# Kernel tuning notes

Hardware: AMD Instinct MI355X
Metric: run time of the kernel (lower is better)

Reference implementation:

```python
import jax, jax.numpy as jnp
import numpy as np

B, T, C, H = 4, 2048, 1024, 16
D = C // H  # head dim = 64


def setup_inputs() -> dict:
    key = jax.random.key(0)
    ks = jax.random.split(key, 5)
    s = 1.0 / np.sqrt(C)
    return {
        "x": jax.random.normal(ks[0], (B, T, C), jnp.float32),
        "Wq": jax.random.normal(ks[1], (C, C), jnp.float32) * s,
        "bq": jnp.zeros((C,), jnp.float32),
        "Wk": jax.random.normal(ks[2], (C, C), jnp.float32) * s,
        "bk": jnp.zeros((C,), jnp.float32),
        "Wv": jax.random.normal(ks[3], (C, C), jnp.float32) * s,
        "bv": jnp.zeros((C,), jnp.float32),
        "Wp": jax.random.normal(ks[4], (C, C), jnp.float32) * s,
        "bp": jnp.zeros((C,), jnp.float32),
    }


def reference(x, Wq, bq, Wk, bk, Wv, bv, Wp, bp):
    # linear projections -> [B, H, T, D]
    def heads(t):
        return t.reshape(B, T, H, D).transpose(0, 2, 1, 3)
    q = heads(x @ Wq.T + bq)
    k = heads(x @ Wk.T + bk)
    v = heads(x @ Wv.T + bv)
    scale = 1.0 / np.sqrt(D)
    att = jnp.einsum("bhtd,bhsd->bhts", q, k) * scale  # [B,H,T,T]
    causal = jnp.tril(jnp.ones((T, T), bool))
    att = jnp.where(causal[None, None], att, -jnp.inf)
    att = jax.nn.softmax(att, axis=-1)
    y = jnp.einsum("bhts,bhsd->bhtd", att, v)  # [B,H,T,D]
    y = y.transpose(0, 2, 1, 3).reshape(B, T, C)
    return y @ Wp.T + bp
```

## Files before the change

kernel.cpp:

```cpp
#include <hip/hip_runtime.h>

typedef float f32x4 __attribute__((ext_vector_type(4)));
typedef float f32x16 __attribute__((ext_vector_type(16)));
typedef __bf16 bf16x8 __attribute__((ext_vector_type(8)));
typedef unsigned short u16x8 __attribute__((ext_vector_type(8)));

#define SCQ 0.1803368801111183f

__device__ inline unsigned short f2bf(float f) {
  unsigned int u = __builtin_bit_cast(unsigned int, f);
  u += 0x7FFFu + ((u >> 16) & 1u);
  return (unsigned short)(u >> 16);
}
__device__ inline unsigned short f2bf_fast(float f) {
  unsigned int u = __builtin_bit_cast(unsigned int, f);
  return (unsigned short)((u + 0x8000u) >> 16);
}

__device__ inline float fexp2(float x) {
#if __has_builtin(__builtin_amdgcn_exp2f)
  return __builtin_amdgcn_exp2f(x);
#else
  return exp2f(x);
#endif
}

template <int N>
__device__ inline float rowror(float v) {
  return __builtin_bit_cast(float, __builtin_amdgcn_update_dpp(
      0, __builtin_bit_cast(int, v), 0x120 | N, 0xF, 0xF, true));
}
__device__ inline float rowsum16(float v) {
  v += rowror<8>(v); v += rowror<4>(v);
  v += rowror<2>(v); v += rowror<1>(v);
  return v;
}

__device__ inline void gload_lds16(const unsigned short* g, unsigned short* l) {
  __builtin_amdgcn_global_load_lds(
      (const __attribute__((address_space(1))) unsigned int*)g,
      (__attribute__((address_space(3))) unsigned int*)l, 16, 0, 0);
}

__global__ void cvt_x(const float* __restrict__ in, unsigned short* __restrict__ out) {
  int i = (blockIdx.x * 256 + threadIdx.x) * 4;
  float4 f = *(const float4*)(in + i);
  ushort4 o;
  o.x = f2bf(f.x); o.y = f2bf(f.y); o.z = f2bf(f.z); o.w = f2bf(f.w);
  *(ushort4*)(out + i) = o;
}

__global__ void cvt_w(const float* __restrict__ a, const float* __restrict__ b,
                      const float* __restrict__ c, const float* __restrict__ d,
                      unsigned short* __restrict__ oa, unsigned short* __restrict__ ob,
                      unsigned short* __restrict__ oc, unsigned short* __restrict__ od) {
  const float* src[4] = {a, b, c, d};
  unsigned short* dst[4] = {oa, ob, oc, od};
  int m = blockIdx.y;
  int i = (blockIdx.x * 256 + threadIdx.x) * 4;
  float4 f = *(const float4*)(src[m] + i);
  ushort4 o;
  o.x = f2bf(f.x); o.y = f2bf(f.y); o.z = f2bf(f.z); o.w = f2bf(f.w);
  *(ushort4*)(dst[m] + i) = o;
}

template <int MODE>
__global__ __launch_bounds__(256) void gemm128(const unsigned short* __restrict__ A,
                                               const unsigned short* __restrict__ Bt,
                                               const float* __restrict__ b0,
                                               const float* __restrict__ b1,
                                               const float* __restrict__ b2,
                                               void* __restrict__ out,
                                               int M, int N, int K) {
  __shared__ __align__(16) unsigned short As[128 * 64];
  __shared__ __align__(16) unsigned short Bs[128 * 64];
  const int tid = threadIdx.x;
  const int lane = tid & 63, w = tid >> 6;
  const int l31 = lane & 31, half = lane >> 5;
  const int wm = w & 1, wn = w >> 1;
  const int m0 = blockIdx.x * 128, n0 = blockIdx.y * 128;

  f32x16 acc[2][2] = {};

  for (int kb = 0; kb < K; kb += 64) {
#pragma unroll
    for (int j = 0; j < 4; j++) {
      int ch = j * 256 + w * 64 + lane;
      int row = ch >> 3, pc = ch & 7;
      int c = pc ^ (row & 7);
      gload_lds16(A + (size_t)(m0 + row) * K + kb + c * 8, As + (size_t)(j * 256 + w * 64) * 8);
      gload_lds16(Bt + (size_t)(n0 + row) * K + kb + c * 8, Bs + (size_t)(j * 256 + w * 64) * 8);
    }
    __syncthreads();
#pragma unroll
    for (int ks = 0; ks < 64; ks += 16) {
      bf16x8 af[2], bfr[2];
#pragma unroll
      for (int at = 0; at < 2; at++) {
        int row = wm * 64 + at * 32 + l31;
        int pc = ((ks >> 3) + half) ^ (row & 7);
        af[at] = *(const bf16x8*)(As + row * 64 + pc * 8);
      }
#pragma unroll
      for (int nt = 0; nt < 2; nt++) {
        int row = wn * 64 + nt * 32 + l31;
        int pc = ((ks >> 3) + half) ^ (row & 7);
        bfr[nt] = *(const bf16x8*)(Bs + row * 64 + pc * 8);
      }
#pragma unroll
      for (int at = 0; at < 2; at++)
#pragma unroll
        for (int nt = 0; nt < 2; nt++)
          acc[at][nt] = __builtin_amdgcn_mfma_f32_32x32x16_bf16(af[at], bfr[nt], acc[at][nt], 0, 0, 0);
    }
    __syncthreads();
  }

#pragma unroll
  for (int at = 0; at < 2; at++)
#pragma unroll
    for (int nt = 0; nt < 2; nt++) {
      int col = n0 + wn * 64 + nt * 32 + l31;
      float bv, sc;
      int which = 0, cl = col;
      if (MODE == 0) {
        which = col >> 10; cl = col & 1023;
        const float* bp = (which == 0) ? b0 : ((which == 1) ? b1 : b2);
        bv = bp[cl];
        sc = (which == 0) ? SCQ : 1.f;
      } else {
        bv = b0[col]; sc = 1.f;
      }
#pragma unroll
      for (int reg = 0; reg < 16; reg++) {
        int row = m0 + wm * 64 + at * 32 + (reg & 3) + 8 * (reg >> 2) + 4 * half;
        float v = (acc[at][nt][reg] + bv) * sc;
        if (MODE == 0) {
          int h = cl >> 6, d = cl & 63;
          int b = row >> 11, t = row & 2047;
          ((unsigned short*)out)[(size_t)which * 8388608 +
                                 ((size_t)((b * 16 + h) * 2048 + t)) * 64 + d] = f2bf(v);
        } else {
          ((float*)out)[(size_t)row * N + col] = v;
        }
      }
    }
}

__global__ __launch_bounds__(256) void transpose_v(const unsigned short* __restrict__ V,
                                                   unsigned short* __restrict__ Vt) {
  constexpr int P = 66;
  __shared__ unsigned short L[64 * P];
  const int tid = threadIdx.x;
  const int bh = blockIdx.y;
  const int t0 = blockIdx.x * 64;
  const unsigned short* Vp = V + (size_t)bh * 2048 * 64;
  unsigned short* Op = Vt + (size_t)bh * 64 * 2048;
#pragma unroll
  for (int j = 0; j < 2; j++) {
    int r = (tid >> 3) + j * 32;
    int c = (tid & 7) * 8;
    u16x8 v = *(const u16x8*)(Vp + (size_t)(t0 + r) * 64 + c);
#pragma unroll
    for (int i = 0; i < 4; i++) {
      unsigned int pk = (unsigned int)v[2 * i] | ((unsigned int)v[2 * i + 1] << 16);
      *(unsigned int*)&L[r * P + c + 2 * i] = pk;
    }
  }
  __syncthreads();
#pragma unroll
  for (int j = 0; j < 2; j++) {
    int ch = j * 256 + tid;
    int d = ch >> 3, tc = (ch & 7) * 8;
    u16x8 o;
#pragma unroll
    for (int k = 0; k < 8; k++) o[k] = L[(tc + k) * P + d];
    *(u16x8*)(Op + (size_t)d * 2048 + t0 + tc) = o;
  }
}

#define PPITCH 72
__device__ __attribute__((always_inline)) inline
void attn_tile(int qt, int s0, const bf16x8* aq, const unsigned short* Ks,
               const unsigned short* Vs, unsigned short* pl,
               f32x4* o, float* lrow, int quad, int l15) {
  const bool full = (s0 + 63) <= qt;
  const int nsc = full ? 4 : (((qt + 15 - s0) >> 4) + 1);
  const int nsc2 = (nsc + 1) & ~1;

#pragma unroll
  for (int sc = 0; sc < 4; sc++) {
    if (sc < nsc) {
      f32x4 s = {};
#pragma unroll
      for (int kh = 0; kh < 2; kh++) {
        int kr = sc * 16 + l15;
        int pc = (kh * 4 + quad) ^ (kr & 7);
        u16x8 bku = *(const u16x8*)(Ks + kr * 64 + pc * 8);
        s = __builtin_amdgcn_mfma_f32_16x16x32_bf16(aq[kh], __builtin_bit_cast(bf16x8, bku), s, 0, 0, 0);
      }
      if (full) {
#pragma unroll
        for (int r = 0; r < 4; r++) {
          float e = fexp2(s[r]);
          lrow[r] += e;
          pl[(quad * 4 + r) * PPITCH + sc * 16 + l15] = f2bf_fast(e);
        }
      } else {
        int sg = s0 + sc * 16 + l15;
#pragma unroll
        for (int r = 0; r < 4; r++) {
          float e = fexp2(s[r]);
          e = (sg > qt + quad * 4 + r) ? 0.f : e;
          lrow[r] += e;
          pl[(quad * 4 + r) * PPITCH + sc * 16 + l15] = f2bf_fast(e);
        }
      }
    } else if (sc < nsc2) {
#pragma unroll
      for (int r = 0; r < 4; r++)
        pl[(quad * 4 + r) * PPITCH + sc * 16 + l15] = 0;
    }
  }
  __asm__ __volatile__("" ::: "memory");
#pragma unroll
  for (int h2 = 0; h2 < 2; h2++) {
    if (h2 * 2 < nsc2) {
      u16x8 apu = *(const u16x8*)(pl + l15 * PPITCH + h2 * 32 + quad * 8);
      bf16x8 ap = __builtin_bit_cast(bf16x8, apu);
#pragma unroll
      for (int dc = 0; dc < 4; dc++) {
        int vr = dc * 16 + l15;
        int pc = (h2 * 4 + quad) ^ (vr & 7);
        u16x8 vu = *(const u16x8*)(Vs + vr * 64 + pc * 8);
        o[dc] = __builtin_amdgcn_mfma_f32_16x16x32_bf16(ap, __builtin_bit_cast(bf16x8, vu), o[dc], 0, 0, 0);
      }
    }
  }
}

__global__ __launch_bounds__(256, 4) void attn_kernel(const unsigned short* __restrict__ Q,
                                                      const unsigned short* __restrict__ Km,
                                                      const unsigned short* __restrict__ Vt,
                                                      unsigned short* __restrict__ Y) {
  constexpr int T = 2048, D = 64;
  __shared__ __align__(16) unsigned short Ks[64 * 64];
  __shared__ __align__(16) unsigned short Vs[64 * 64];
  __shared__ __align__(16) unsigned short P_lds[4][16 * PPITCH];
  const int tid = threadIdx.x;
  const int lane = tid & 63, w = tid >> 6;
  const int quad = lane >> 4, l15 = lane & 15;
  const int bh = blockIdx.x;
  const int b = bh >> 4, h = bh & 15;
  const int p = blockIdx.y;
  const unsigned short* Qp = Q + (size_t)bh * T * D;
  const unsigned short* Kp = Km + (size_t)bh * T * D;
  const unsigned short* Vp = Vt + (size_t)bh * D * T;
  unsigned short* pl = P_lds[w];

  const int bch0 = (w * 2) * 64, bch1 = (w * 2 + 1) * 64;
  const int ch0 = bch0 + lane, ch1 = bch1 + lane;
  const int row0 = ch0 >> 3, c0 = (ch0 & 7) ^ (row0 & 7);
  const int row1 = ch1 >> 3, c1 = (ch1 & 7) ^ (row1 & 7);

  for (int phase = 0; phase < 2; ++phase) {
    const int jt = phase ? (127 - (p * 4 + w)) : (p * 4 + w);
    const int qt = jt * 16;
    const int nit = phase ? (32 - p) : (p + 1);

    bf16x8 aq[2];
    aq[0] = *(const bf16x8*)(Qp + (size_t)(qt + l15) * D + quad * 8);
    aq[1] = *(const bf16x8*)(Qp + (size_t)(qt + l15) * D + 32 + quad * 8);

    f32x4 o[4] = {};
    float lrow[4] = {0.f, 0.f, 0.f, 0.f};

    for (int it = 0; it < nit; ++it) {
      const int s0 = it * 64;
      gload_lds16(Kp + (size_t)(s0 + row0) * 64 + c0 * 8, Ks + (size_t)bch0 * 8);
      gload_lds16(Kp + (size_t)(s0 + row1) * 64 + c1 * 8, Ks + (size_t)bch1 * 8);
      gload_lds16(Vp + (size_t)row0 * T + s0 + c0 * 8, Vs + (size_t)bch0 * 8);
      gload_lds16(Vp + (size_t)row1 * T + s0 + c1 * 8, Vs + (size_t)bch1 * 8);
      __syncthreads();

      attn_tile(qt, s0, aq, Ks, Vs, pl, o, lrow, quad, l15);

      __syncthreads();
    }

#pragma unroll
    for (int r = 0; r < 4; r++) {
      float inv = 1.f / rowsum16(lrow[r]);
      int qg = qt + quad * 4 + r;
#pragma unroll
      for (int dc = 0; dc < 4; dc++)
        Y[((size_t)(b * T + qg)) * 1024 + h * 64 + dc * 16 + l15] = f2bf(o[dc][r] * inv);
    }
  }
}

extern "C" void kernel_launch(void* const* d_in, const int* in_sizes, int n_in,
                              void* d_out, int out_size, void* d_ws, size_t ws_size,
                              hipStream_t stream) {
  const float* x  = (const float*)d_in[0];
  const float* Wq = (const float*)d_in[1];
  const float* bq = (const float*)d_in[2];
  const float* Wk = (const float*)d_in[3];
  const float* bk = (const float*)d_in[4];
  const float* Wv = (const float*)d_in[5];
  const float* bv = (const float*)d_in[6];
  const float* Wp = (const float*)d_in[7];
  const float* bp = (const float*)d_in[8];

  char* ws = (char*)d_ws;
  unsigned short* xb  = (unsigned short*)(ws + 0);
  unsigned short* wqb = (unsigned short*)(ws + 16777216);
  unsigned short* wkb = (unsigned short*)(ws + 18874368);
  unsigned short* wvb = (unsigned short*)(ws + 20971520);
  unsigned short* wpb = (unsigned short*)(ws + 23068672);
  unsigned short* Qb  = (unsigned short*)(ws + 25165824);
  unsigned short* Kb  = (unsigned short*)(ws + 41943040);
  unsigned short* Vb  = (unsigned short*)(ws + 58720256);
  unsigned short* Vtb = xb;
  unsigned short* Yb  = Vb;

  cvt_x<<<8192, 256, 0, stream>>>(x, xb);
  cvt_w<<<dim3(1024, 4), 256, 0, stream>>>(Wq, Wk, Wv, Wp, wqb, wkb, wvb, wpb);

  gemm128<0><<<dim3(64, 24), 256, 0, stream>>>(xb, wqb, bq, bk, bv, Qb, 8192, 3072, 1024);

  transpose_v<<<dim3(32, 64), 256, 0, stream>>>(Vb, Vtb);
  attn_kernel<<<dim3(64, 16), 256, 0, stream>>>(Qb, Kb, Vtb, Yb);

  gemm128<1><<<dim3(64, 8), 256, 0, stream>>>(Yb, wpb, bp, bp, bp, d_out, 8192, 1024, 1024);
}
```

Baseline: 253.9 us.

## Double-buffer K/V tiles in attention and swizzle P scratch layout

Adds a second LDS buffer for K and V so the next 64-key tile is prefetched with async global-to-LDS loads while the current tile is computed. Explicit vmcnt waits and raw s_barriers replace the __syncthreads pair. The per-wave P scratch also changes from a padded pitch-72 layout to an XOR-swizzled pitch-64 layout to avoid bank conflicts. The extra buffers double the K/V LDS footprint, which may limit occupancy, and the hand-written waitcnt logic is fragile.

```diff
diff --git a/kernel.cpp b/kernel.cpp
--- a/kernel.cpp
+++ b/kernel.cpp
@@ -179,7 +179,6 @@
   }
 }
 
-#define PPITCH 72
 __device__ __attribute__((always_inline)) inline
 void attn_tile(int qt, int s0, const bf16x8* aq, const unsigned short* Ks,
                const unsigned short* Vs, unsigned short* pl,
@@ -187,6 +186,7 @@
   const bool full = (s0 + 63) <= qt;
   const int nsc = full ? 4 : (((qt + 15 - s0) >> 4) + 1);
   const int nsc2 = (nsc + 1) & ~1;
+  const int pb = l15 >> 3, pp = l15 & 7;
 
 #pragma unroll
   for (int sc = 0; sc < 4; sc++) {
@@ -204,7 +204,8 @@
         for (int r = 0; r < 4; r++) {
           float e = fexp2(s[r]);
           lrow[r] += e;
-          pl[(quad * 4 + r) * PPITCH + sc * 16 + l15] = f2bf_fast(e);
+          int prow = quad * 4 + r;
+          pl[prow * 64 + (((sc * 2 + pb) ^ (prow & 7)) << 3) + pp] = f2bf_fast(e);
         }
       } else {
         int sg = s0 + sc * 16 + l15;
@@ -213,20 +214,23 @@
           float e = fexp2(s[r]);
           e = (sg > qt + quad * 4 + r) ? 0.f : e;
           lrow[r] += e;
-          pl[(quad * 4 + r) * PPITCH + sc * 16 + l15] = f2bf_fast(e);
+          int prow = quad * 4 + r;
+          pl[prow * 64 + (((sc * 2 + pb) ^ (prow & 7)) << 3) + pp] = f2bf_fast(e);
         }
       }
     } else if (sc < nsc2) {
 #pragma unroll
-      for (int r = 0; r < 4; r++)
-        pl[(quad * 4 + r) * PPITCH + sc * 16 + l15] = 0;
+      for (int r = 0; r < 4; r++) {
+        int prow = quad * 4 + r;
+        pl[prow * 64 + (((sc * 2 + pb) ^ (prow & 7)) << 3) + pp] = 0;
+      }
     }
   }
   __asm__ __volatile__("" ::: "memory");
 #pragma unroll
   for (int h2 = 0; h2 < 2; h2++) {
     if (h2 * 2 < nsc2) {
-      u16x8 apu = *(const u16x8*)(pl + l15 * PPITCH + h2 * 32 + quad * 8);
+      u16x8 apu = *(const u16x8*)(pl + l15 * 64 + (((h2 * 4 + quad) ^ (l15 & 7)) << 3));
       bf16x8 ap = __builtin_bit_cast(bf16x8, apu);
 #pragma unroll
       for (int dc = 0; dc < 4; dc++) {
@@ -244,9 +248,9 @@
                                                       const unsigned short* __restrict__ Vt,
                                                       unsigned short* __restrict__ Y) {
   constexpr int T = 2048, D = 64;
-  __shared__ __align__(16) unsigned short Ks[64 * 64];
-  __shared__ __align__(16) unsigned short Vs[64 * 64];
-  __shared__ __align__(16) unsigned short P_lds[4][16 * PPITCH];
+  __shared__ __align__(16) unsigned short Ks[2][64 * 64];
+  __shared__ __align__(16) unsigned short Vs[2][64 * 64];
+  __shared__ __align__(16) unsigned short P_lds[4][16 * 64];
   const int tid = threadIdx.x;
   const int lane = tid & 63, w = tid >> 6;
   const int quad = lane >> 4, l15 = lane & 15;
@@ -271,21 +275,40 @@
     bf16x8 aq[2];
     aq[0] = *(const bf16x8*)(Qp + (size_t)(qt + l15) * D + quad * 8);
     aq[1] = *(const bf16x8*)(Qp + (size_t)(qt + l15) * D + 32 + quad * 8);
+    __asm__ __volatile__("" :: "v"(__builtin_bit_cast(f32x4, aq[0])),
+                              "v"(__builtin_bit_cast(f32x4, aq[1])));
 
     f32x4 o[4] = {};
     float lrow[4] = {0.f, 0.f, 0.f, 0.f};
 
+    gload_lds16(Kp + (size_t)row0 * 64 + c0 * 8, Ks[0] + bch0 * 8);
+    gload_lds16(Kp + (size_t)row1 * 64 + c1 * 8, Ks[0] + bch1 * 8);
+    gload_lds16(Vp + (size_t)row0 * T + c0 * 8, Vs[0] + bch0 * 8);
+    gload_lds16(Vp + (size_t)row1 * T + c1 * 8, Vs[0] + bch1 * 8);
+
+    int cur = 0;
     for (int it = 0; it < nit; ++it) {
       const int s0 = it * 64;
-      gload_lds16(Kp + (size_t)(s0 + row0) * 64 + c0 * 8, Ks + (size_t)bch0 * 8);
-      gload_lds16(Kp + (size_t)(s0 + row1) * 64 + c1 * 8, Ks + (size_t)bch1 * 8);
-      gload_lds16(Vp + (size_t)row0 * T + s0 + c0 * 8, Vs + (size_t)bch0 * 8);
-      gload_lds16(Vp + (size_t)row1 * T + s0 + c1 * 8, Vs + (size_t)bch1 * 8);
-      __syncthreads();
-
-      attn_tile(qt, s0, aq, Ks, Vs, pl, o, lrow, quad, l15);
-
-      __syncthreads();
+      if (it + 1 < nit) {
+        const int s1 = s0 + 64;
+        unsigned short* kd = Ks[cur ^ 1];
+        unsigned short* vd = Vs[cur ^ 1];
+        gload_lds16(Kp + (size_t)(s1 + row0) * 64 + c0 * 8, kd + bch0 * 8);
+        gload_lds16(Kp + (size_t)(s1 + row1) * 64 + c1 * 8, kd + bch1 * 8);
+        gload_lds16(Vp + (size_t)row0 * T + s1 + c0 * 8, vd + bch0 * 8);
+        gload_lds16(Vp + (size_t)row1 * T + s1 + c1 * 8, vd + bch1 * 8);
+        __asm__ __volatile__("s_waitcnt vmcnt(4)" ::: "memory");
+      } else {
+        __asm__ __volatile__("s_waitcnt vmcnt(0)" ::: "memory");
+      }
+      __builtin_amdgcn_s_barrier();
+      __builtin_amdgcn_sched_barrier(0);
+
+      attn_tile(qt, s0, aq, Ks[cur], Vs[cur], pl, o, lrow, quad, l15);
+
+      __builtin_amdgcn_sched_barrier(0);
+      __builtin_amdgcn_s_barrier();
+      cur ^= 1;
     }
 
 #pragma unroll
```

Measured after the change: 259.0 us. 1.02x slower.
